# Performance work log

Measured on AMD Instinct MI355X. Metric: run time of the kernel, lower is better.

## Reference

```python
import jax, jax.numpy as jnp
import numpy as np

N = 50000      # nodes
E = 800000     # edges
F_NODE = 64
PE = 16
F_EDGE = 16
H = 128        # hidden_dim
L = 4          # num_layers
G = 64         # graphs in batch
NC = 10        # num_classes
BN_EPS = 1e-5


def _bn(h, g, b):
    # BatchNorm1d with batch statistics (deterministic train-style stats, no dropout)
    m = jnp.mean(h, axis=0)
    v = jnp.var(h, axis=0)
    return (h - m) * jax.lax.rsqrt(v + BN_EPS) * g + b


def setup_inputs() -> dict:
    key = jax.random.key(0)
    ks = jax.random.split(key, 16)
    p = lambda k, shape: (jax.random.normal(k, shape, jnp.float32) * 0.05)
    return dict(
        x=jax.random.normal(ks[0], (N, F_NODE), jnp.float32),
        pe=jax.random.normal(ks[1], (N, PE), jnp.float32),
        edge_index=jax.random.randint(ks[2], (2, E), 0, N),
        edge_attr=jax.random.normal(ks[3], (E, F_EDGE), jnp.float32),
        batch=jnp.sort(jax.random.randint(ks[4], (N,), 0, G)),
        W_in=p(ks[5], (F_NODE + PE, H)), b_in=jnp.zeros((H,), jnp.float32),
        We_edge=p(ks[6], (L, F_EDGE, H)), be_edge=jnp.zeros((L, H), jnp.float32),
        eps=jnp.zeros((L,), jnp.float32),
        W1_gin=p(ks[7], (L, H, 2 * H)), b1_gin=jnp.zeros((L, 2 * H), jnp.float32),
        W2_gin=p(ks[8], (L, 2 * H, H)), b2_gin=jnp.zeros((L, H), jnp.float32),
        bn1_g=jnp.ones((L, H), jnp.float32), bn1_b=jnp.zeros((L, H), jnp.float32),
        W1_ffn=p(ks[9], (L, H, 2 * H)), b1_ffn=jnp.zeros((L, 2 * H), jnp.float32),
        W2_ffn=p(ks[10], (L, 2 * H, H)), b2_ffn=jnp.zeros((L, H), jnp.float32),
        bn2_g=jnp.ones((L, H), jnp.float32), bn2_b=jnp.zeros((L, H), jnp.float32),
        W_r1=p(ks[11], (H, H)), b_r1=jnp.zeros((H,), jnp.float32),
        W_r2=p(ks[12], (H, NC)), b_r2=jnp.zeros((NC,), jnp.float32),
    )


def reference(x, pe, edge_index, edge_attr, batch,
              W_in, b_in, We_edge, be_edge, eps,
              W1_gin, b1_gin, W2_gin, b2_gin, bn1_g, bn1_b,
              W1_ffn, b1_ffn, W2_ffn, b2_ffn, bn2_g, bn2_b,
              W_r1, b_r1, W_r2, b_r2):
    src, dst = edge_index[0], edge_index[1]  # PyG: row=source j, col=target i
    # input projection on [x || pe]
    h = jax.nn.relu(jnp.concatenate([x, pe], axis=-1) @ W_in + b_in)  # [N,H]
    for l in range(L):
        # --- GINEConv: msg = relu(x_j + lin_edge(e_ij)); sum-aggregate to target
        e = edge_attr @ We_edge[l] + be_edge[l]                        # [E,H]
        msg = jax.nn.relu(h[src] + e)                                  # gather + fuse
        agg = jax.ops.segment_sum(msg, dst, num_segments=N)           # scatter-add
        z = (1.0 + eps[l]) * h + agg
        z = jax.nn.relu(z @ W1_gin[l] + b1_gin[l]) @ W2_gin[l] + b2_gin[l]
        # --- GNNPlusLayer: BN -> ReLU -> residual (identity proj, in==out)
        z = jax.nn.relu(_bn(z, bn1_g[l], bn1_b[l]))
        z = z + h
        # --- FFN (eval mode): out = lin2(relu(lin1(z))) + z, then BN
        f = jax.nn.relu(z @ W1_ffn[l] + b1_ffn[l]) @ W2_ffn[l] + b2_ffn[l]
        h = _bn(f + z, bn2_g[l], bn2_b[l])
    # --- global mean pool over graphs
    sums = jax.ops.segment_sum(h, batch, num_segments=G)               # [G,H]
    counts = jax.ops.segment_sum(jnp.ones((N,), h.dtype), batch, num_segments=G)
    hg = sums / jnp.maximum(counts, 1.0)[:, None]
    # --- readout MLP (dropout off in eval)
    return jax.nn.relu(hg @ W_r1 + b_r1) @ W_r2 + b_r2                 # [G,NC]
```

## Files before the change

kernel.cpp:

```cpp
#include <hip/hip_runtime.h>
#include <hip/hip_bf16.h>

#define NN 50000
#define NE 800000
#define FIN 80
#define H 128
#define H2 256
#define NG 64
#define NCLS 10
#define BN_EPS 1e-5f
#define NB 196

typedef __attribute__((ext_vector_type(8))) short bf16x8;
typedef __attribute__((ext_vector_type(8))) unsigned short us8;
typedef __attribute__((ext_vector_type(4))) float f32x4;

__device__ __forceinline__ unsigned short f2b(float f) {
    __hip_bfloat16 h = __float2bfloat16(f);
    return *(unsigned short*)&h;
}
__device__ __forceinline__ float b2f(unsigned short u) {
    unsigned v = (unsigned)u << 16;
    return __uint_as_float(v);
}

__global__ void wprep_kernel(const float* __restrict__ W, unsigned short* __restrict__ Wt,
                             int K, int Nn)
{
    const int idx = blockIdx.x * 256 + threadIdx.x;
    const int per = K * Nn;
    const int l = idx / per;
    const int r = idx - l * per;
    const int k = r / Nn;
    const int n = r - k * Nn;
    const float wv = W[idx];
    const unsigned short hi = f2b(wv);
    const unsigned short lo = f2b(wv - b2f(hi));
    const int KB = K >> 5;
    const int kb = k >> 5, kk = k & 31;
    unsigned short* base = Wt + (size_t)l * 2 * per;
    base[((size_t)(0 * KB + kb) * Nn + n) * 32 + kk] = hi;
    base[((size_t)(1 * KB + kb) * Nn + n) * 32 + kk] = lo;
}

template<bool ABF, bool CBF, bool ZF>
__global__ __launch_bounds__(256, 2)
void mgemm(const void* __restrict__ Ap, const unsigned short* __restrict__ Wt,
           const float* __restrict__ bias, const float* __restrict__ resid,
           void* __restrict__ Cp, int M, int K, int Nn, int relu,
           float* __restrict__ statsOut,
           const float* __restrict__ statsIn, const float* __restrict__ bng,
           const float* __restrict__ bnb, const float* __restrict__ hres,
           float* __restrict__ zout, float inv_n)
{
    __shared__ unsigned short sA[128][32];
    __shared__ unsigned short sB[2][128][32];
    __shared__ float sAB[128];
    __shared__ float sSH[128];

    const int tid = threadIdx.x;
    const int m0 = blockIdx.x * 128;
    const int n0 = blockIdx.y * 128;
    const int lane = tid & 63;
    const int w = tid >> 6;
    const int KB = K >> 5;

    if (ZF) {
        if (tid < 128) {
            const float mean = statsIn[tid] * inv_n;
            const float var = statsIn[128 + tid] * inv_n - mean * mean;
            const float a = bng[tid] * rsqrtf(var + BN_EPS);
            sAB[tid] = a;
            sSH[tid] = fmaf(-mean, a, bnb[tid]);
        }
    }

    f32x4 acc[2][8];
#pragma unroll
    for (int r = 0; r < 2; ++r)
#pragma unroll
        for (int c = 0; c < 8; ++c) acc[r][c] = (f32x4)(0.f);

    const int arow = tid >> 1;
    const int akh = (tid & 1) * 16;
    const int gm = m0 + arow;
    const int fr = lane & 15;
    const int fq = (lane >> 4) * 8;

    for (int kb = 0; kb < KB; ++kb) {
        const int k0 = kb * 32;
        __syncthreads();
        if (ABF) {
            if (gm < M) {
                const unsigned short* Ab = (const unsigned short*)Ap + (size_t)gm * K + k0 + akh;
                *(float4*)&sA[arow][akh]     = *(const float4*)Ab;
                *(float4*)&sA[arow][akh + 8] = *(const float4*)(Ab + 8);
            } else {
                *(float4*)&sA[arow][akh]     = make_float4(0.f, 0.f, 0.f, 0.f);
                *(float4*)&sA[arow][akh + 8] = make_float4(0.f, 0.f, 0.f, 0.f);
            }
        } else if (ZF) {
            if (gm < M) {
                const float* tf = (const float*)Ap + (size_t)gm * K + k0 + akh;
                const float* hf = hres + (size_t)gm * K + k0 + akh;
                float zv[16];
#pragma unroll
                for (int i = 0; i < 16; ++i) {
                    const int c = k0 + akh + i;
                    zv[i] = fmaxf(fmaf(tf[i], sAB[c], sSH[c]), 0.f) + hf[i];
                }
                if (blockIdx.y == 0) {
                    float* zo = zout + (size_t)gm * K + k0 + akh;
#pragma unroll
                    for (int i = 0; i < 16; i += 4)
                        *(float4*)(zo + i) = make_float4(zv[i], zv[i + 1], zv[i + 2], zv[i + 3]);
                }
                us8 p0, p1;
#pragma unroll
                for (int i = 0; i < 8; ++i) { p0[i] = f2b(zv[i]); p1[i] = f2b(zv[8 + i]); }
                *(us8*)&sA[arow][akh]     = p0;
                *(us8*)&sA[arow][akh + 8] = p1;
            } else {
                *(float4*)&sA[arow][akh]     = make_float4(0.f, 0.f, 0.f, 0.f);
                *(float4*)&sA[arow][akh + 8] = make_float4(0.f, 0.f, 0.f, 0.f);
            }
        } else {
            if (gm < M) {
                const float* Af = (const float*)Ap + (size_t)gm * K + k0 + akh;
                const float4 v0 = *(const float4*)(Af);
                const float4 v1 = *(const float4*)(Af + 4);
                const float4 v2 = *(const float4*)(Af + 8);
                const float4 v3 = *(const float4*)(Af + 12);
                const float vals[16] = {v0.x, v0.y, v0.z, v0.w, v1.x, v1.y, v1.z, v1.w,
                                        v2.x, v2.y, v2.z, v2.w, v3.x, v3.y, v3.z, v3.w};
                us8 p0, p1;
#pragma unroll
                for (int i = 0; i < 8; ++i) { p0[i] = f2b(vals[i]); p1[i] = f2b(vals[8 + i]); }
                *(us8*)&sA[arow][akh]     = p0;
                *(us8*)&sA[arow][akh + 8] = p1;
            } else {
                *(float4*)&sA[arow][akh]     = make_float4(0.f, 0.f, 0.f, 0.f);
                *(float4*)&sA[arow][akh + 8] = make_float4(0.f, 0.f, 0.f, 0.f);
            }
        }
#pragma unroll
        for (int p = 0; p < 2; ++p) {
            const unsigned short* src = Wt + ((size_t)(p * KB + kb) * Nn + n0) * 32 + tid * 16;
            unsigned short* dst = &sB[p][0][0] + tid * 16;
            *(float4*)dst       = *(const float4*)src;
            *(float4*)(dst + 8) = *(const float4*)(src + 8);
        }
        __syncthreads();
        const bf16x8 a0 = *(const bf16x8*)&sA[w * 32 + fr][fq];
        const bf16x8 a1 = *(const bf16x8*)&sA[w * 32 + 16 + fr][fq];
#pragma unroll
        for (int c = 0; c < 8; ++c) {
            const bf16x8 bh = *(const bf16x8*)&sB[0][c * 16 + fr][fq];
            const bf16x8 bl = *(const bf16x8*)&sB[1][c * 16 + fr][fq];
            acc[0][c] = __builtin_amdgcn_mfma_f32_16x16x32_bf16(a0, bh, acc[0][c], 0, 0, 0);
            acc[0][c] = __builtin_amdgcn_mfma_f32_16x16x32_bf16(a0, bl, acc[0][c], 0, 0, 0);
            acc[1][c] = __builtin_amdgcn_mfma_f32_16x16x32_bf16(a1, bh, acc[1][c], 0, 0, 0);
            acc[1][c] = __builtin_amdgcn_mfma_f32_16x16x32_bf16(a1, bl, acc[1][c], 0, 0, 0);
        }
    }

    float s[8], q[8];
#pragma unroll
    for (int c = 0; c < 8; ++c) { s[c] = 0.f; q[c] = 0.f; }
    const int crow4 = (lane >> 4) * 4;
#pragma unroll
    for (int r = 0; r < 2; ++r) {
        const int rbase = m0 + w * 32 + r * 16 + crow4;
#pragma unroll
        for (int c = 0; c < 8; ++c) {
            const int gc = n0 + c * 16 + fr;
            const float bb = bias[gc];
#pragma unroll
            for (int reg = 0; reg < 4; ++reg) {
                const int gr = rbase + reg;
                if (gr >= M) continue;
                float o = acc[r][c][reg] + bb;
                if (resid) o += resid[(size_t)gr * Nn + gc];
                if (relu) o = fmaxf(o, 0.f);
                if (statsOut) { s[c] += o; q[c] = fmaf(o, o, q[c]); }
                if (CBF) ((unsigned short*)Cp)[(size_t)gr * Nn + gc] = f2b(o);
                else     ((float*)Cp)[(size_t)gr * Nn + gc] = o;
            }
        }
    }

    if (statsOut) {
#pragma unroll
        for (int c = 0; c < 8; ++c) {
            s[c] += __shfl_xor(s[c], 32, 64); s[c] += __shfl_xor(s[c], 16, 64);
            q[c] += __shfl_xor(q[c], 32, 64); q[c] += __shfl_xor(q[c], 16, 64);
        }
        __syncthreads();
        float* red = (float*)sA;
        if (lane < 16) {
#pragma unroll
            for (int c = 0; c < 8; ++c) {
                red[w * 128 + c * 16 + lane]       = s[c];
                red[512 + w * 128 + c * 16 + lane] = q[c];
            }
        }
        __syncthreads();
        if (tid < 128) {
            const float ss = red[tid] + red[128 + tid] + red[256 + tid] + red[384 + tid];
            const float qq = red[512 + tid] + red[640 + tid] + red[768 + tid] + red[896 + tid];
            atomicAdd(&statsOut[tid], ss);
            atomicAdd(&statsOut[128 + tid], qq);
        }
    }
}

__global__ __launch_bounds__(256, 4)
void inproj_kernel(const float* __restrict__ x, const float* __restrict__ pe,
                   const float* __restrict__ W, const float* __restrict__ bias,
                   float* __restrict__ C, unsigned short* __restrict__ Cb, int M)
{
    __shared__ float aT[16][128];
    __shared__ float wsh[16][128];

    const int tid = threadIdx.x;
    const int m0 = blockIdx.x * 128;
    const int rm = (tid >> 4) * 8;
    const int rn = (tid & 15) * 8;

    float acc[8][8];
#pragma unroll
    for (int i = 0; i < 8; ++i)
#pragma unroll
        for (int j = 0; j < 8; ++j) acc[i][j] = 0.f;

    const int lm = tid & 127;
    const int kq = (tid >> 7) * 8;
    const int wk = tid >> 4;
    const int wj = (tid & 15) * 8;

    for (int k0 = 0; k0 < FIN; k0 += 16) {
        {
            const int gm = m0 + lm;
            const int c = k0 + kq;
            if (gm < M) {
                const float* srcp = (c < 64) ? (x + (size_t)gm * 64 + c)
                                             : (pe + (size_t)gm * 16 + (c - 64));
                const float4 v0 = *(const float4*)srcp;
                const float4 v1 = *(const float4*)(srcp + 4);
                aT[kq + 0][lm] = v0.x; aT[kq + 1][lm] = v0.y;
                aT[kq + 2][lm] = v0.z; aT[kq + 3][lm] = v0.w;
                aT[kq + 4][lm] = v1.x; aT[kq + 5][lm] = v1.y;
                aT[kq + 6][lm] = v1.z; aT[kq + 7][lm] = v1.w;
            } else {
#pragma unroll
                for (int i = 0; i < 8; ++i) aT[kq + i][lm] = 0.f;
            }
        }
        {
            const float4 w0 = *(const float4*)&W[(size_t)(k0 + wk) * H + wj];
            const float4 w1 = *(const float4*)&W[(size_t)(k0 + wk) * H + wj + 4];
            *(float4*)&wsh[wk][wj]     = w0;
            *(float4*)&wsh[wk][wj + 4] = w1;
        }
        __syncthreads();
#pragma unroll
        for (int k = 0; k < 16; ++k) {
            const float4 a0 = *(const float4*)&aT[k][rm];
            const float4 a1 = *(const float4*)&aT[k][rm + 4];
            const float4 b0 = *(const float4*)&wsh[k][rn];
            const float4 b1 = *(const float4*)&wsh[k][rn + 4];
            const float av[8] = {a0.x, a0.y, a0.z, a0.w, a1.x, a1.y, a1.z, a1.w};
            const float bv[8] = {b0.x, b0.y, b0.z, b0.w, b1.x, b1.y, b1.z, b1.w};
#pragma unroll
            for (int i = 0; i < 8; ++i)
#pragma unroll
                for (int j = 0; j < 8; ++j)
                    acc[i][j] = fmaf(av[i], bv[j], acc[i][j]);
        }
        __syncthreads();
    }

    float bv[8];
#pragma unroll
    for (int j = 0; j < 8; ++j) bv[j] = bias[rn + j];
#pragma unroll
    for (int i = 0; i < 8; ++i) {
        const int gm = m0 + rm + i;
        if (gm >= M) continue;
        float o[8];
#pragma unroll
        for (int j = 0; j < 8; ++j) o[j] = fmaxf(acc[i][j] + bv[j], 0.f);
        *(float4*)&C[(size_t)gm * H + rn]     = make_float4(o[0], o[1], o[2], o[3]);
        *(float4*)&C[(size_t)gm * H + rn + 4] = make_float4(o[4], o[5], o[6], o[7]);
        us8 pk;
#pragma unroll
        for (int j = 0; j < 8; ++j) pk[j] = f2b(o[j]);
        *(us8*)&Cb[(size_t)gm * H + rn] = pk;
    }
}

__global__ void hist_kernel(const int* __restrict__ ei, int* __restrict__ deg)
{
    const int e = blockIdx.x * 256 + threadIdx.x;
    if (e < NE) atomicAdd(&deg[ei[NE + e]], 1);
}

__global__ void bsum_kernel(const int* __restrict__ deg, int* __restrict__ bsum)
{
    const int tid = threadIdx.x;
    const int i = blockIdx.x * 256 + tid;
    int v = (i < NN) ? deg[i] : 0;
#pragma unroll
    for (int off = 32; off > 0; off >>= 1) v += __shfl_down(v, off, 64);
    __shared__ int ws[4];
    if ((tid & 63) == 0) ws[tid >> 6] = v;
    __syncthreads();
    if (tid == 0) bsum[blockIdx.x] = ws[0] + ws[1] + ws[2] + ws[3];
}

__global__ void bscan_kernel(int* __restrict__ bsum)
{
    __shared__ int sh[256];
    const int tid = threadIdx.x;
    sh[tid] = (tid < NB) ? bsum[tid] : 0;
    __syncthreads();
    for (int off = 1; off < 256; off <<= 1) {
        const int t = (tid >= off) ? sh[tid - off] : 0;
        __syncthreads();
        sh[tid] += t;
        __syncthreads();
    }
    if (tid < NB) bsum[tid] = (tid == 0) ? 0 : sh[tid - 1];
}

__global__ void bwrite_kernel(const int* __restrict__ deg, const int* __restrict__ boff,
                              int* __restrict__ rowptr, int* __restrict__ cursor)
{
    __shared__ int sh[256];
    const int tid = threadIdx.x;
    const int i = blockIdx.x * 256 + tid;
    const int v = (i < NN) ? deg[i] : 0;
    sh[tid] = v;
    __syncthreads();
    for (int off = 1; off < 256; off <<= 1) {
        const int t = (tid >= off) ? sh[tid - off] : 0;
        __syncthreads();
        sh[tid] += t;
        __syncthreads();
    }
    if (i < NN) {
        const int pos = boff[blockIdx.x] + sh[tid] - v;
        rowptr[i] = pos;
        cursor[i] = pos;
    }
    if (blockIdx.x == 0 && tid == 0) rowptr[NN] = NE;
}

__global__ void scatter_kernel(const int* __restrict__ ei, const float* __restrict__ ea,
                               int* __restrict__ cursor, int* __restrict__ src_s,
                               float* __restrict__ ea_s)
{
    const int e = blockIdx.x * 256 + threadIdx.x;
    if (e >= NE) return;
    const int d = ei[NE + e];
    const int pos = atomicAdd(&cursor[d], 1);
    src_s[pos] = ei[e];
    const float4* sp = (const float4*)&ea[(size_t)e * 16];
    float4* dp = (float4*)&ea_s[(size_t)pos * 16];
    dp[0] = sp[0]; dp[1] = sp[1]; dp[2] = sp[2]; dp[3] = sp[3];
}

__global__ __launch_bounds__(256)
void agg_kernel(const float* __restrict__ h, const unsigned short* __restrict__ hb,
                const int* __restrict__ rowptr, const int* __restrict__ src_s,
                const float* __restrict__ ea_s, const float* __restrict__ We,
                const float* __restrict__ be, const float* __restrict__ eps, int l,
                float* __restrict__ z)
{
    const int lane = threadIdx.x & 63;
    const int w = threadIdx.x >> 6;
    const int n = blockIdx.x * 4 + w;
    if (n >= NN) return;

    float w0[16], w1[16];
#pragma unroll
    for (int k = 0; k < 16; ++k) {
        const float2 wv = *(const float2*)&We[k * H + 2 * lane];
        w0[k] = wv.x; w1[k] = wv.y;
    }
    const float2 bev = *(const float2*)&be[2 * lane];

    const int beg = __builtin_amdgcn_readfirstlane(rowptr[n]);
    const int end = __builtin_amdgcn_readfirstlane(rowptr[n + 1]);

    const float e1 = 1.0f + eps[l];
    const float2 hv0 = *(const float2*)&h[(size_t)n * H + 2 * lane];
    float acc0 = e1 * hv0.x;
    float acc1 = e1 * hv0.y;

    for (int i0 = beg; i0 < end; i0 += 8) {
        const int jn = min(8, end - i0);
        int srcs[8];
#pragma unroll
        for (int j = 0; j < 8; ++j)
            srcs[j] = src_s[(i0 + j < end) ? (i0 + j) : (end - 1)];
        unsigned hraw[8];
#pragma unroll
        for (int j = 0; j < 8; ++j)
            hraw[j] = *(const unsigned*)&hb[(size_t)srcs[j] * H + 2 * lane];
#pragma unroll
        for (int j = 0; j < 8; ++j) {
            if (j >= jn) break;
            const float* ar = ea_s + (size_t)(i0 + j) * 16;
            float s0 = bev.x, s1 = bev.y;
#pragma unroll
            for (int k = 0; k < 16; ++k) {
                const float a = ar[k];
                s0 = fmaf(a, w0[k], s0);
                s1 = fmaf(a, w1[k], s1);
            }
            const float hx = __uint_as_float(hraw[j] << 16);
            const float hy = __uint_as_float(hraw[j] & 0xffff0000u);
            acc0 += fmaxf(hx + s0, 0.f);
            acc1 += fmaxf(hy + s1, 0.f);
        }
    }
    *(float2*)&z[(size_t)n * H + 2 * lane] = make_float2(acc0, acc1);
}

__global__ void bn_apply_kernel(const float* __restrict__ u, const float* __restrict__ st,
                                const float* __restrict__ g, const float* __restrict__ b,
                                float* __restrict__ h, unsigned short* __restrict__ hb,
                                float inv_n)
{
    const int i = blockIdx.x * 256 + threadIdx.x;
    const int c = i & (H - 1);
    const float mean = st[c] * inv_n;
    const float var = st[H + c] * inv_n - mean * mean;
    const float a = g[c] * rsqrtf(var + BN_EPS);
    const float s = fmaf(-mean, a, b[c]);
    const float v = fmaf(u[i], a, s);
    h[i] = v;
    hb[i] = f2b(v);
}

__global__ void pool_kernel(const float* __restrict__ h, const int* __restrict__ batch,
                            float* __restrict__ pool, float* __restrict__ cnt, int n)
{
    const int c = threadIdx.x & (H - 1);
    const int half = threadIdx.x >> 7;
    const int r0 = blockIdx.x * 256 + half * 128;
    if (r0 >= n) return;
    const int rend = min(r0 + 128, n);
    int gprev = batch[r0];
    float acc = 0.f;
    int run = 0;
    for (int r = r0; r < rend; ++r) {
        const int g = batch[r];
        if (g != gprev) {
            atomicAdd(&pool[gprev * H + c], acc);
            if (c == 0) atomicAdd(&cnt[gprev], (float)run);
            acc = 0.f; run = 0; gprev = g;
        }
        acc += h[(size_t)r * H + c];
        run++;
    }
    atomicAdd(&pool[gprev * H + c], acc);
    if (c == 0) atomicAdd(&cnt[gprev], (float)run);
}

__global__ void readout_kernel(const float* __restrict__ pool, const float* __restrict__ cnt,
                               const float* __restrict__ Wr1, const float* __restrict__ br1,
                               const float* __restrict__ Wr2, const float* __restrict__ br2,
                               float* __restrict__ out)
{
    __shared__ float hg[H];
    __shared__ float r1[H];
    const int g = blockIdx.x;
    const int j = threadIdx.x;
    hg[j] = pool[g * H + j] / fmaxf(cnt[g], 1.0f);
    __syncthreads();
    float acc = br1[j];
    for (int k = 0; k < H; ++k) acc = fmaf(hg[k], Wr1[k * H + j], acc);
    r1[j] = fmaxf(acc, 0.f);
    __syncthreads();
    if (j < NCLS) {
        float o = br2[j];
        for (int k = 0; k < H; ++k) o = fmaf(r1[k], Wr2[k * NCLS + j], o);
        out[g * NCLS + j] = o;
    }
}

extern "C" void kernel_launch(void* const* d_in, const int* in_sizes, int n_in,
                              void* d_out, int out_size, void* d_ws, size_t ws_size,
                              hipStream_t stream)
{
    const float* x       = (const float*)d_in[0];
    const float* pe      = (const float*)d_in[1];
    const int*   ei      = (const int*)d_in[2];
    const float* ea      = (const float*)d_in[3];
    const int*   batch   = (const int*)d_in[4];
    const float* W_in    = (const float*)d_in[5];
    const float* b_in    = (const float*)d_in[6];
    const float* We_edge = (const float*)d_in[7];
    const float* be_edge = (const float*)d_in[8];
    const float* eps     = (const float*)d_in[9];
    const float* W1g     = (const float*)d_in[10];
    const float* b1g     = (const float*)d_in[11];
    const float* W2g     = (const float*)d_in[12];
    const float* b2g     = (const float*)d_in[13];
    const float* bn1g    = (const float*)d_in[14];
    const float* bn1b    = (const float*)d_in[15];
    const float* W1f     = (const float*)d_in[16];
    const float* b1f     = (const float*)d_in[17];
    const float* W2f     = (const float*)d_in[18];
    const float* b2f     = (const float*)d_in[19];
    const float* bn2g    = (const float*)d_in[20];
    const float* bn2b    = (const float*)d_in[21];
    const float* Wr1     = (const float*)d_in[22];
    const float* br1     = (const float*)d_in[23];
    const float* Wr2     = (const float*)d_in[24];
    const float* br2     = (const float*)d_in[25];
    float* out = (float*)d_out;

    const size_t NH = (size_t)NN * H;
    float* hbuf  = (float*)d_ws;
    float* zbuf  = hbuf + NH;
    float* tbuf  = zbuf + NH;
    unsigned short* z1 = (unsigned short*)(tbuf + NH);
    float* stats = (float*)(z1 + (size_t)NN * H2);
    float* pool  = stats + 2048;
    float* cnt   = pool + NG * H;
    int*   rowptr = (int*)(cnt + NG);
    int*   cursor = rowptr + NN + 1;
    int*   deg    = cursor + NN;
    int*   bsum   = deg + NN;
    int*   src_s  = bsum + 256;
    float* ea_s   = (float*)(src_s + NE);
    unsigned short* hb = (unsigned short*)(ea_s + (size_t)NE * 16);
    unsigned short* wt = hb + NH;
    unsigned short* wt1g = wt;
    unsigned short* wt2g = wt + 4 * 65536;
    unsigned short* wt1f = wt + 8 * 65536;
    unsigned short* wt2f = wt + 12 * 65536;

    const dim3 blk(256);
    const dim3 mg1((NN + 127) / 128, 1);
    const dim3 mg2((NN + 127) / 128, 2);
    const int ew_grid = (int)(NH / 256);
    const float inv_n = 1.0f / (float)NN;

    wprep_kernel<<<512, blk, 0, stream>>>(W1g, wt1g, 128, 256);
    wprep_kernel<<<512, blk, 0, stream>>>(W2g, wt2g, 256, 128);
    wprep_kernel<<<512, blk, 0, stream>>>(W1f, wt1f, 128, 256);
    wprep_kernel<<<512, blk, 0, stream>>>(W2f, wt2f, 256, 128);

    hipMemsetAsync(deg, 0, NN * sizeof(int), stream);
    hipMemsetAsync(stats, 0, 2048 * sizeof(float), stream);
    hist_kernel<<<(NE + 255) / 256, blk, 0, stream>>>(ei, deg);
    bsum_kernel<<<NB, blk, 0, stream>>>(deg, bsum);
    bscan_kernel<<<1, blk, 0, stream>>>(bsum);
    bwrite_kernel<<<NB, blk, 0, stream>>>(deg, bsum, rowptr, cursor);
    scatter_kernel<<<(NE + 255) / 256, blk, 0, stream>>>(ei, ea, cursor, src_s, ea_s);

    inproj_kernel<<<mg1, blk, 0, stream>>>(x, pe, W_in, b_in, hbuf, hb, NN);

    for (int l = 0; l < 4; ++l) {
        float* s1 = stats + (size_t)l * 512;
        float* s2 = s1 + 256;

        agg_kernel<<<(NN + 3) / 4, blk, 0, stream>>>(hbuf, hb, rowptr, src_s, ea_s,
                                                     We_edge + (size_t)l * 16 * H,
                                                     be_edge + (size_t)l * H, eps, l, zbuf);

        mgemm<false, true, false><<<mg2, blk, 0, stream>>>(
            zbuf, wt1g + (size_t)l * 65536, b1g + (size_t)l * H2, nullptr, z1,
            NN, 128, 256, 1, nullptr, nullptr, nullptr, nullptr, nullptr, nullptr, inv_n);
        mgemm<true, false, false><<<mg1, blk, 0, stream>>>(
            z1, wt2g + (size_t)l * 65536, b2g + (size_t)l * H, nullptr, tbuf,
            NN, 256, 128, 0, s1, nullptr, nullptr, nullptr, nullptr, nullptr, inv_n);

        mgemm<false, true, true><<<mg2, blk, 0, stream>>>(
            tbuf, wt1f + (size_t)l * 65536, b1f + (size_t)l * H2, nullptr, z1,
            NN, 128, 256, 1, nullptr, s1, bn1g + (size_t)l * H, bn1b + (size_t)l * H,
            hbuf, zbuf, inv_n);

        mgemm<true, false, false><<<mg1, blk, 0, stream>>>(
            z1, wt2f + (size_t)l * 65536, b2f + (size_t)l * H, zbuf, tbuf,
            NN, 256, 128, 0, s2, nullptr, nullptr, nullptr, nullptr, nullptr, inv_n);

        bn_apply_kernel<<<ew_grid, blk, 0, stream>>>(tbuf, s2, bn2g + (size_t)l * H,
                                                     bn2b + (size_t)l * H, hbuf, hb, inv_n);
    }

    hipMemsetAsync(pool, 0, (NG * H + NG) * sizeof(float), stream);
    pool_kernel<<<(NN + 255) / 256, blk, 0, stream>>>(hbuf, batch, pool, cnt, NN);
    readout_kernel<<<NG, H, 0, stream>>>(pool, cnt, Wr1, br1, Wr2, br2, out);
}
```

Measured before the change: 1.329 ms.

## Pad shared tiles to avoid bank conflicts and merge prep launches and memsets

Pads the GEMM shared-memory A/B tiles to a row stride of 40 halfwords and remaps the weight-tile copy to the padded layout, with the aim of reducing LDS bank conflicts on MFMA fragment reads. Pads the input-projection shared tiles to 129 floats and swaps their vector loads and stores for scalar ones. Merges the four weight-prep launches into one kernel and moves buffers so that a single memset zeroes degrees, stats and pool. The padding costs a little more LDS and the scalar accesses add more instructions.

Measured after the change: 1.319 ms. No clear change (-0.8%).

```diff
diff --git a/kernel.cpp b/kernel.cpp
--- a/kernel.cpp
+++ b/kernel.cpp
@@ -10,6 +10,7 @@
 #define NCLS 10
 #define BN_EPS 1e-5f
 #define NB 196
+#define LDK 40
 
 typedef __attribute__((ext_vector_type(8))) short bf16x8;
 typedef __attribute__((ext_vector_type(8))) unsigned short us8;
@@ -24,16 +25,26 @@
     return __uint_as_float(v);
 }
 
-__global__ void wprep_kernel(const float* __restrict__ W, unsigned short* __restrict__ Wt,
-                             int K, int Nn)
+__global__ void wprep_all(const float* __restrict__ W1g, const float* __restrict__ W2g,
+                          const float* __restrict__ W1f, const float* __restrict__ W2f,
+                          unsigned short* __restrict__ wt)
 {
     const int idx = blockIdx.x * 256 + threadIdx.x;
+    const int m = idx >> 17;
+    const int r = idx & 131071;
+    const float* W;
+    unsigned short* Wt;
+    int K, Nn;
+    if (m == 0)      { W = W1g; Wt = wt;              K = 128; Nn = 256; }
+    else if (m == 1) { W = W2g; Wt = wt + 4 * 65536;  K = 256; Nn = 128; }
+    else if (m == 2) { W = W1f; Wt = wt + 8 * 65536;  K = 128; Nn = 256; }
+    else             { W = W2f; Wt = wt + 12 * 65536; K = 256; Nn = 128; }
     const int per = K * Nn;
-    const int l = idx / per;
-    const int r = idx - l * per;
-    const int k = r / Nn;
-    const int n = r - k * Nn;
-    const float wv = W[idx];
+    const int l = r / per;
+    const int rr = r - l * per;
+    const int k = rr / Nn;
+    const int n = rr - k * Nn;
+    const float wv = W[r];
     const unsigned short hi = f2b(wv);
     const unsigned short lo = f2b(wv - b2f(hi));
     const int KB = K >> 5;
@@ -53,8 +64,8 @@
            const float* __restrict__ bnb, const float* __restrict__ hres,
            float* __restrict__ zout, float inv_n)
 {
-    __shared__ unsigned short sA[128][32];
-    __shared__ unsigned short sB[2][128][32];
+    __shared__ unsigned short sA[128][LDK];
+    __shared__ unsigned short sB[2][128][LDK];
     __shared__ float sAB[128];
     __shared__ float sSH[128];
 
@@ -145,10 +156,11 @@
         }
 #pragma unroll
         for (int p = 0; p < 2; ++p) {
-            const unsigned short* src = Wt + ((size_t)(p * KB + kb) * Nn + n0) * 32 + tid * 16;
-            unsigned short* dst = &sB[p][0][0] + tid * 16;
-            *(float4*)dst       = *(const float4*)src;
-            *(float4*)(dst + 8) = *(const float4*)(src + 8);
+            const int bn = tid >> 1;
+            const int bkh = (tid & 1) * 16;
+            const unsigned short* src = Wt + ((size_t)(p * KB + kb) * Nn + n0 + bn) * 32 + bkh;
+            *(float4*)&sB[p][bn][bkh]     = *(const float4*)src;
+            *(float4*)&sB[p][bn][bkh + 8] = *(const float4*)(src + 8);
         }
         __syncthreads();
         const bf16x8 a0 = *(const bf16x8*)&sA[w * 32 + fr][fq];
@@ -219,8 +231,8 @@
                    const float* __restrict__ W, const float* __restrict__ bias,
                    float* __restrict__ C, unsigned short* __restrict__ Cb, int M)
 {
-    __shared__ float aT[16][128];
-    __shared__ float wsh[16][128];
+    __shared__ float aT[16][129];
+    __shared__ float wsh[16][129];
 
     const int tid = threadIdx.x;
     const int m0 = blockIdx.x * 128;
@@ -257,20 +269,17 @@
             }
         }
         {
-            const float4 w0 = *(const float4*)&W[(size_t)(k0 + wk) * H + wj];
-            const float4 w1 = *(const float4*)&W[(size_t)(k0 + wk) * H + wj + 4];
-            *(float4*)&wsh[wk][wj]     = w0;
-            *(float4*)&wsh[wk][wj + 4] = w1;
+#pragma unroll
+            for (int j = 0; j < 8; ++j)
+                wsh[wk][wj + j] = W[(size_t)(k0 + wk) * H + wj + j];
         }
         __syncthreads();
 #pragma unroll
         for (int k = 0; k < 16; ++k) {
-            const float4 a0 = *(const float4*)&aT[k][rm];
-            const float4 a1 = *(const float4*)&aT[k][rm + 4];
-            const float4 b0 = *(const float4*)&wsh[k][rn];
-            const float4 b1 = *(const float4*)&wsh[k][rn + 4];
-            const float av[8] = {a0.x, a0.y, a0.z, a0.w, a1.x, a1.y, a1.z, a1.w};
-            const float bv[8] = {b0.x, b0.y, b0.z, b0.w, b1.x, b1.y, b1.z, b1.w};
+            const float av[8] = {aT[k][rm], aT[k][rm + 1], aT[k][rm + 2], aT[k][rm + 3],
+                                 aT[k][rm + 4], aT[k][rm + 5], aT[k][rm + 6], aT[k][rm + 7]};
+            const float bv[8] = {wsh[k][rn], wsh[k][rn + 1], wsh[k][rn + 2], wsh[k][rn + 3],
+                                 wsh[k][rn + 4], wsh[k][rn + 5], wsh[k][rn + 6], wsh[k][rn + 7]};
 #pragma unroll
             for (int i = 0; i < 8; ++i)
 #pragma unroll
@@ -528,13 +537,13 @@
     float* zbuf  = hbuf + NH;
     float* tbuf  = zbuf + NH;
     unsigned short* z1 = (unsigned short*)(tbuf + NH);
-    float* stats = (float*)(z1 + (size_t)NN * H2);
+    int*   deg   = (int*)(z1 + (size_t)NN * H2);
+    float* stats = (float*)(deg + NN);
     float* pool  = stats + 2048;
     float* cnt   = pool + NG * H;
     int*   rowptr = (int*)(cnt + NG);
     int*   cursor = rowptr + NN + 1;
-    int*   deg    = cursor + NN;
-    int*   bsum   = deg + NN;
+    int*   bsum   = cursor + NN;
     int*   src_s  = bsum + 256;
     float* ea_s   = (float*)(src_s + NE);
     unsigned short* hb = (unsigned short*)(ea_s + (size_t)NE * 16);
@@ -549,14 +558,11 @@
     const dim3 mg2((NN + 127) / 128, 2);
     const int ew_grid = (int)(NH / 256);
     const float inv_n = 1.0f / (float)NN;
-
-    wprep_kernel<<<512, blk, 0, stream>>>(W1g, wt1g, 128, 256);
-    wprep_kernel<<<512, blk, 0, stream>>>(W2g, wt2g, 256, 128);
-    wprep_kernel<<<512, blk, 0, stream>>>(W1f, wt1f, 128, 256);
-    wprep_kernel<<<512, blk, 0, stream>>>(W2f, wt2f, 256, 128);
-
-    hipMemsetAsync(deg, 0, NN * sizeof(int), stream);
-    hipMemsetAsync(stats, 0, 2048 * sizeof(float), stream);
+    const size_t zero_bytes = (size_t)(NN + 2048 + NG * H + NG) * 4;
+
+    wprep_all<<<2048, blk, 0, stream>>>(W1g, W2g, W1f, W2f, wt);
+
+    hipMemsetAsync(deg, 0, zero_bytes, stream);
     hist_kernel<<<(NE + 255) / 256, blk, 0, stream>>>(ei, deg);
     bsum_kernel<<<NB, blk, 0, stream>>>(deg, bsum);
     bscan_kernel<<<1, blk, 0, stream>>>(bsum);
@@ -593,7 +599,6 @@
                                                      bn2b + (size_t)l * H, hbuf, hb, inv_n);
     }
 
-    hipMemsetAsync(pool, 0, (NG * H + NG) * sizeof(float), stream);
     pool_kernel<<<(NN + 255) / 256, blk, 0, stream>>>(hbuf, batch, pool, cnt, NN);
     readout_kernel<<<NG, H, 0, stream>>>(pool, cnt, Wr1, br1, Wr2, br2, out);
 }
```
